# Kernel tuning notes

Hardware: AMD Instinct MI355X
Metric: run time of the kernel (lower is better)

The kernel has to match this reference:

```python
import jax, jax.numpy as jnp
import numpy as np

D_MODEL = 1024
D_FF = 4096
N_EXPERTS = 8
TOP_K = 2

def setup_inputs() -> dict:
    key = jax.random.key(0)
    ks = jax.random.split(key, 8)
    s = 0.02
    return {
        "x": jax.random.normal(ks[0], (4, 2048, D_MODEL), dtype=jnp.float32),
        "W1": jax.random.normal(ks[1], (N_EXPERTS, D_MODEL, D_FF), dtype=jnp.float32) * s,
        "b1": jnp.zeros((N_EXPERTS, D_FF), dtype=jnp.float32),
        "W2": jax.random.normal(ks[2], (N_EXPERTS, D_FF, D_MODEL), dtype=jnp.float32) * s,
        "b2": jnp.zeros((N_EXPERTS, D_MODEL), dtype=jnp.float32),
        "Wg": jax.random.normal(ks[3], (D_MODEL, N_EXPERTS), dtype=jnp.float32) * s,
        "bg": jnp.zeros((N_EXPERTS,), dtype=jnp.float32),
    }

def reference(x, W1, b1, W2, b2, Wg, bg):
    B, S, D = x.shape
    # Gating network
    gate_logits = jnp.einsum('bsd,de->bse', x, Wg) + bg
    gate_probs = jax.nn.softmax(gate_logits, axis=-1)  # (B,S,E)
    # Top-k routing on softmax probs (matches torch.topk(F.softmax(logits)))
    top_k_probs, top_k_indices = jax.lax.top_k(gate_probs, TOP_K)  # (B,S,k)
    T = B * S
    x_flat = x.reshape(T, D)
    idx_flat = top_k_indices.reshape(T, TOP_K)
    prob_flat = top_k_probs.reshape(T, TOP_K)
    # Per-token combine weight for each expert: sum of top-k probs routed to it
    # combine[t, e] = sum_j prob_flat[t, j] * (idx_flat[t, j] == e)
    onehot = jax.nn.one_hot(idx_flat, N_EXPERTS, dtype=x.dtype)  # (T,k,E)
    combine = jnp.einsum('tk,tke->te', prob_flat, onehot)  # (T,E)
    out = jnp.zeros((T, D), dtype=x.dtype)
    for e in range(N_EXPERTS):  # static small loop over experts
        h = jax.nn.relu(x_flat @ W1[e] + b1[e])  # (T, d_ff)
        y = h @ W2[e] + b2[e]                    # (T, d_model)
        out = out + combine[:, e:e+1] * y
    return out.reshape(B, S, D), gate_probs
```

## Files before the change

kernel.cpp:

```cpp
#include <hip/hip_runtime.h>

#define D_MODEL 1024
#define D_FF    4096
#define N_EXP   8
#define BM 128
#define BN 128
#define BK 32

typedef __attribute__((ext_vector_type(8))) short bf16x8;
typedef __attribute__((ext_vector_type(4))) float f32x4;
typedef unsigned int u32;

__device__ __forceinline__ unsigned short f2bf(float f) {
  union { float f; unsigned u; } v; v.f = f;
  unsigned r = v.u + 0x7FFFu + ((v.u >> 16) & 1u);
  return (unsigned short)(r >> 16);
}

__device__ __forceinline__ void gl_lds16(const void* g, void* l) {
  __builtin_amdgcn_global_load_lds((const __attribute__((address_space(1))) u32*)g,
                                   (__attribute__((address_space(3))) u32*)l, 16, 0, 0);
}

__global__ __launch_bounds__(256)
void transpose_convert_all(const float* __restrict__ W1, const float* __restrict__ W2,
                           unsigned short* __restrict__ w1t, unsigned short* __restrict__ w2t) {
  __shared__ u32 s32k[32][65];
  int z = blockIdx.z;
  const float* se;
  unsigned short* de;
  int Ksub, Nsrc, kb, nb;
  if (z < 8) {
    Ksub = D_MODEL; Nsrc = D_FF;
    kb = blockIdx.y * 64; nb = blockIdx.x * 64;
    se = W1 + (size_t)z * D_MODEL * D_FF;
    de = w1t + (size_t)z * D_FF * D_MODEL;
  } else {
    Ksub = D_FF; Nsrc = D_MODEL;
    kb = blockIdx.x * 64; nb = blockIdx.y * 64;
    se = W2 + (size_t)(z - 8) * D_FF * D_MODEL;
    de = w2t + (size_t)(z - 8) * D_MODEL * D_FF;
  }
  se += (size_t)kb * Nsrc + nb;
  de += (size_t)nb * Ksub + kb;
  int tid = threadIdx.x;
  int kh = tid >> 4;
  int n4 = (tid & 15) * 4;
  #pragma unroll
  for (int p = 0; p < 2; p++) {
    int k = kh * 2 + p * 32;
    float4 v0 = *(const float4*)(se + (size_t)k * Nsrc + n4);
    float4 v1 = *(const float4*)(se + (size_t)(k + 1) * Nsrc + n4);
    #pragma unroll
    for (int j = 0; j < 4; j++) {
      u32 pk = (u32)f2bf(((const float*)&v0)[j]) |
               ((u32)f2bf(((const float*)&v1)[j]) << 16);
      s32k[k >> 1][n4 + j] = pk;
    }
  }
  __syncthreads();
  #pragma unroll
  for (int c = 0; c < 2; c++) {
    int id = tid + c * 256;
    int n = id >> 3, kc = id & 7;
    uint4 o;
    o.x = s32k[kc * 4 + 0][n];
    o.y = s32k[kc * 4 + 1][n];
    o.z = s32k[kc * 4 + 2][n];
    o.w = s32k[kc * 4 + 3][n];
    *(uint4*)(de + (size_t)n * Ksub + kc * 8) = o;
  }
}

__global__ void gating_kernel(const float* __restrict__ x,
                              const float* __restrict__ Wg,
                              const float* __restrict__ bg,
                              float* __restrict__ gate_out,
                              unsigned short* __restrict__ xb,
                              int* __restrict__ cnt,
                              int* __restrict__ tokIdx,
                              float* __restrict__ tokW, int T) {
  int wv = threadIdx.x >> 6, lane = threadIdx.x & 63;
  int t = blockIdx.x * 4 + wv;
  if (t >= T) return;
  const float* xr = x + (size_t)t * D_MODEL + lane * 16;
  float acc[N_EXP];
  #pragma unroll
  for (int e = 0; e < N_EXP; e++) acc[e] = 0.f;
  ushort4 xc[4];
  #pragma unroll
  for (int q = 0; q < 4; q++) {
    float4 xv = *(const float4*)(xr + q * 4);
    xc[q].x = f2bf(xv.x); xc[q].y = f2bf(xv.y);
    xc[q].z = f2bf(xv.z); xc[q].w = f2bf(xv.w);
    #pragma unroll
    for (int r = 0; r < 4; r++) {
      float xs = ((const float*)&xv)[r];
      const float* wrow = Wg + (size_t)(lane * 16 + q * 4 + r) * N_EXP;
      float4 wa = *(const float4*)wrow;
      float4 wb = *(const float4*)(wrow + 4);
      acc[0] += xs * wa.x; acc[1] += xs * wa.y; acc[2] += xs * wa.z; acc[3] += xs * wa.w;
      acc[4] += xs * wb.x; acc[5] += xs * wb.y; acc[6] += xs * wb.z; acc[7] += xs * wb.w;
    }
  }
  unsigned short* xbr = xb + (size_t)t * D_MODEL + lane * 16;
  #pragma unroll
  for (int q = 0; q < 4; q++) *(ushort4*)(xbr + q * 4) = xc[q];
  #pragma unroll
  for (int off = 32; off > 0; off >>= 1) {
    #pragma unroll
    for (int e = 0; e < N_EXP; e++) acc[e] += __shfl_xor(acc[e], off);
  }
  if (lane == 0) {
    float l[N_EXP], p[N_EXP];
    float m = -1e30f;
    #pragma unroll
    for (int e = 0; e < N_EXP; e++) { l[e] = acc[e] + bg[e]; m = fmaxf(m, l[e]); }
    float s = 0.f;
    #pragma unroll
    for (int e = 0; e < N_EXP; e++) { p[e] = __expf(l[e] - m); s += p[e]; }
    float inv = 1.f / s;
    #pragma unroll
    for (int e = 0; e < N_EXP; e++) { p[e] *= inv; gate_out[(size_t)t * N_EXP + e] = p[e]; }
    int e1 = 0;
    #pragma unroll
    for (int e = 1; e < N_EXP; e++) if (p[e] > p[e1]) e1 = e;
    int e2 = (e1 == 0) ? 1 : 0;
    #pragma unroll
    for (int e = 0; e < N_EXP; e++) if (e != e1 && p[e] > p[e2]) e2 = e;
    int pos = atomicAdd(cnt + e1, 1);
    tokIdx[(size_t)e1 * T + pos] = t; tokW[(size_t)e1 * T + pos] = p[e1];
    pos = atomicAdd(cnt + e2, 1);
    tokIdx[(size_t)e2 * T + pos] = t; tokW[(size_t)e2 * T + pos] = p[e2];
  }
}

__global__ void schedule_kernel(const int* __restrict__ cnt, int* __restrict__ meta,
                                int* __restrict__ tE, int* __restrict__ tB,
                                int* __restrict__ tV, int T, int maxTiles) {
  if (threadIdx.x != 0 || blockIdx.x != 0) return;
  int t = 0;
  for (int e = 0; e < N_EXP; e++) {
    int c = cnt[e];
    for (int r = 0; r < c && t < maxTiles; r += BM) {
      tE[t] = e; tB[t] = e * T + r; tV[t] = min(BM, c - r); t++;
    }
  }
  meta[0] = t;
}

#define STAGE(b, kt) { _Pragma("unroll") for (int p_ = 0; p_ < 2; p_++) { \
    gl_lds16(srcA[p_] + (size_t)(kt) * BK, &LDSU[(b) * 8192 + (w * 32 + p_ * 16) * 32]); \
    gl_lds16(srcB[p_] + (size_t)(kt) * BK, &LDSU[(b) * 8192 + 4096 + (w * 32 + p_ * 16) * 32]); } }

#define COMPUTE(b) { \
    bf16x8 ra[4], rb[4]; \
    _Pragma("unroll") for (int m_ = 0; m_ < 4; m_++) { \
      int row_ = wr * 64 + m_ * 16 + l15; \
      ra[m_] = *(const bf16x8*)&LDSU[(b) * 8192 + row_ * 32 + (((l4 + (row_ >> 1)) & 3) << 3)]; } \
    _Pragma("unroll") for (int n_ = 0; n_ < 4; n_++) { \
      int rb_ = wc * 64 + n_ * 16 + l15; \
      rb[n_] = *(const bf16x8*)&LDSU[(b) * 8192 + 4096 + rb_ * 32 + (((l4 + (rb_ >> 1)) & 3) << 3)]; } \
    _Pragma("unroll") for (int m_ = 0; m_ < 4; m_++) \
      _Pragma("unroll") for (int n_ = 0; n_ < 4; n_++) \
        acc[m_][n_] = __builtin_amdgcn_mfma_f32_16x16x32_bf16(ra[m_], rb[n_], acc[m_][n_], 0, 0, 0); }

#define BAR() { __builtin_amdgcn_s_barrier(); asm volatile("" ::: "memory"); }
#define WAITVM(N) asm volatile("s_waitcnt vmcnt(" #N ")" ::: "memory");

#define PIPE3(NT) \
  STAGE(0, 0); STAGE(1, 1); \
  for (int it = 0; it < ((NT) - 2) / 3; it++) { \
    int kt = 3 * it; \
    STAGE(2, kt + 2); WAITVM(8); BAR(); COMPUTE(0); BAR(); \
    STAGE(0, kt + 3); WAITVM(8); BAR(); COMPUTE(1); BAR(); \
    STAGE(1, kt + 4); WAITVM(8); BAR(); COMPUTE(2); BAR(); \
  } \
  WAITVM(4); BAR(); COMPUTE(0); BAR(); \
  WAITVM(0); BAR(); COMPUTE(1);

__global__ __launch_bounds__(256)
void gemm1_kernel(const unsigned short* __restrict__ xb,
                  const unsigned short* __restrict__ w1t,
                  const float* __restrict__ b1,
                  const int* __restrict__ meta,
                  const int* __restrict__ tE, const int* __restrict__ tB,
                  const int* __restrict__ tV, const int* __restrict__ tokIdx,
                  unsigned short* __restrict__ h, int nT) {
  __shared__ unsigned short LDSU[24576];

  int total = gridDim.x;
  int L = blockIdx.x;
  int q = total >> 3, r8 = total & 7;
  int xcd = L & 7, idx = L >> 3;
  int work = (xcd < r8) ? (xcd * (q + 1) + idx) : (r8 * (q + 1) + (xcd - r8) * q + idx);
  int cb = work / nT;
  int tile = work - cb * nT;
  if (tile >= meta[0]) return;
  int e = tE[tile], base = tB[tile], valid = tV[tile];
  int tid = threadIdx.x;

  int w = tid >> 6, lane = tid & 63;
  int wr = w >> 1, wc = w & 1;
  int l15 = lane & 15, l4 = lane >> 4;
  int lrow = lane >> 2, lch = lane & 3;

  const unsigned short* panel = w1t + (size_t)e * D_FF * D_MODEL;
  const unsigned short* srcA[2];
  const unsigned short* srcB[2];
  #pragma unroll
  for (int p = 0; p < 2; p++) {
    int r = w * 32 + p * 16 + lrow;
    int tok = tokIdx[base + (r < valid ? r : valid - 1)];
    int g = (lch - (r >> 1)) & 3;
    srcA[p] = xb + (size_t)tok * D_MODEL + g * 8;
    srcB[p] = panel + (size_t)(cb * BN + r) * D_MODEL + g * 8;
  }

  f32x4 acc[4][4];
  #pragma unroll
  for (int m = 0; m < 4; m++)
    #pragma unroll
    for (int n = 0; n < 4; n++) acc[m][n] = (f32x4){0.f, 0.f, 0.f, 0.f};

  PIPE3(D_MODEL / BK);

  #pragma unroll
  for (int n = 0; n < 4; n++) {
    int colc = cb * BN + wc * 64 + n * 16 + l15;
    float bias = b1[(size_t)e * D_FF + colc];
    #pragma unroll
    for (int m = 0; m < 4; m++) {
      #pragma unroll
      for (int r = 0; r < 4; r++) {
        int row = wr * 64 + m * 16 + l4 * 4 + r;
        float v = acc[m][n][r] + bias;
        v = v > 0.f ? v : 0.f;
        h[(size_t)(tile * BM + row) * D_FF + colc] = f2bf(v);
      }
    }
  }
}

__global__ __launch_bounds__(256)
void gemm2_kernel(const unsigned short* __restrict__ h,
                  const unsigned short* __restrict__ w2t,
                  const float* __restrict__ b2,
                  const int* __restrict__ meta,
                  const int* __restrict__ tE, const int* __restrict__ tB,
                  const int* __restrict__ tV, const int* __restrict__ tokIdx,
                  const float* __restrict__ tokW,
                  float* __restrict__ out) {
  __shared__ unsigned short LDSU[24576];

  int total = gridDim.x;
  int L = blockIdx.x;
  int q = total >> 3, r8 = total & 7;
  int xcd = L & 7, idx = L >> 3;
  int work = (xcd < r8) ? (xcd * (q + 1) + idx) : (r8 * (q + 1) + (xcd - r8) * q + idx);
  int tile = work >> 3;
  int cb = work & 7;
  if (tile >= meta[0]) return;
  int e = tE[tile], base = tB[tile], valid = tV[tile];
  int tid = threadIdx.x;

  int w = tid >> 6, lane = tid & 63;
  int wr = w >> 1, wc = w & 1;
  int l15 = lane & 15, l4 = lane >> 4;
  int lrow = lane >> 2, lch = lane & 3;

  const unsigned short* panel = w2t + (size_t)e * D_MODEL * D_FF;
  const unsigned short* srcA[2];
  const unsigned short* srcB[2];
  #pragma unroll
  for (int p = 0; p < 2; p++) {
    int r = w * 32 + p * 16 + lrow;
    int g = (lch - (r >> 1)) & 3;
    srcA[p] = h + (size_t)(tile * BM + r) * D_FF + g * 8;
    srcB[p] = panel + (size_t)(cb * BN + r) * D_FF + g * 8;
  }

  f32x4 acc[4][4];
  #pragma unroll
  for (int m = 0; m < 4; m++)
    #pragma unroll
    for (int n = 0; n < 4; n++) acc[m][n] = (f32x4){0.f, 0.f, 0.f, 0.f};

  PIPE3(D_FF / BK);

  float biasv[4];
  #pragma unroll
  for (int n = 0; n < 4; n++)
    biasv[n] = b2[(size_t)e * D_MODEL + cb * BN + wc * 64 + n * 16 + l15];

  #pragma unroll
  for (int m = 0; m < 4; m++) {
    #pragma unroll
    for (int r = 0; r < 4; r++) {
      int row = wr * 64 + m * 16 + l4 * 4 + r;
      if (row < valid) {
        int tok = tokIdx[base + row];
        float wgt = tokW[base + row];
        float* orow = out + (size_t)tok * D_MODEL + cb * BN + wc * 64 + l15;
        #pragma unroll
        for (int n = 0; n < 4; n++)
          atomicAdd(orow + n * 16, (acc[m][n][r] + biasv[n]) * wgt);
      }
    }
  }
}

extern "C" void kernel_launch(void* const* d_in, const int* in_sizes, int n_in,
                              void* d_out, int out_size, void* d_ws, size_t ws_size,
                              hipStream_t stream) {
  const float* x  = (const float*)d_in[0];
  const float* W1 = (const float*)d_in[1];
  const float* b1 = (const float*)d_in[2];
  const float* W2 = (const float*)d_in[3];
  const float* b2 = (const float*)d_in[4];
  const float* Wg = (const float*)d_in[5];
  const float* bg = (const float*)d_in[6];

  int T = in_sizes[0] / D_MODEL;
  float* out = (float*)d_out;
  float* gate_out = out + (size_t)T * D_MODEL;

  char* ws = (char*)d_ws;
  int* cnt  = (int*)(ws + 0);
  int* meta = (int*)(ws + 64);
  int* tE   = (int*)(ws + 128);
  int* tB   = (int*)(ws + 1024);
  int* tV   = (int*)(ws + 2048);
  size_t off = 4096;
  int* tokIdx = (int*)(ws + off);   off += (size_t)N_EXP * T * 4;
  float* tokW = (float*)(ws + off); off += (size_t)N_EXP * T * 4;
  unsigned short* xb = (unsigned short*)(ws + off); off += (size_t)T * D_MODEL * 2;
  off = (off + 255) & ~(size_t)255;

  int maxTiles = (2 * T) / BM + N_EXP;

  unsigned short* w1t = (unsigned short*)(ws + off); off += (size_t)N_EXP * D_MODEL * D_FF * 2;
  unsigned short* w2t = (unsigned short*)(ws + off); off += (size_t)N_EXP * D_MODEL * D_FF * 2;
  unsigned short* h   = (unsigned short*)(ws + off);

  hipMemsetAsync(d_out, 0, (size_t)T * D_MODEL * sizeof(float), stream);
  hipMemsetAsync(cnt, 0, N_EXP * sizeof(int), stream);

  gating_kernel<<<(T + 3) / 4, 256, 0, stream>>>(x, Wg, bg, gate_out, xb, cnt, tokIdx, tokW, T);
  schedule_kernel<<<1, 64, 0, stream>>>(cnt, meta, tE, tB, tV, T, maxTiles);

  transpose_convert_all<<<dim3(64, 16, 16), 256, 0, stream>>>(W1, W2, w1t, w2t);

  gemm1_kernel<<<maxTiles * (D_FF / BN), 256, 0, stream>>>(
      xb, w1t, b1, meta, tE, tB, tV, tokIdx, h, maxTiles);
  gemm2_kernel<<<maxTiles * (D_MODEL / BN), 256, 0, stream>>>(
      h, w2t, b2, meta, tE, tB, tV, tokIdx, tokW, out);
}
```

Measured before the change: 738.9 us.

## Use 512-thread blocks with 2x4 wave grid for expert GEMMs

Both expert GEMM kernels now run 8 waves per block in a 2x4 arrangement instead of 4 waves in 2x2, so each wave computes a 64x32 sub-tile with half the accumulators. Each thread issues one global-to-LDS load per operand per stage, and the vmcnt waits are adjusted to match. This lowers per-thread register pressure and adds latency hiding within the same 128x128 tile, at the cost of more redundant A-fragment LDS reads per MFMA and heavier barrier synchronization across 8 waves.

```diff
diff --git a/kernel.cpp b/kernel.cpp
--- a/kernel.cpp
+++ b/kernel.cpp
@@ -149,21 +149,21 @@
   meta[0] = t;
 }
 
-#define STAGE(b, kt) { _Pragma("unroll") for (int p_ = 0; p_ < 2; p_++) { \
-    gl_lds16(srcA[p_] + (size_t)(kt) * BK, &LDSU[(b) * 8192 + (w * 32 + p_ * 16) * 32]); \
-    gl_lds16(srcB[p_] + (size_t)(kt) * BK, &LDSU[(b) * 8192 + 4096 + (w * 32 + p_ * 16) * 32]); } }
+#define STAGE(b, kt) { \
+    gl_lds16(srcA0 + (size_t)(kt) * BK, &LDSU[(b) * 8192 + w * 512]); \
+    gl_lds16(srcB0 + (size_t)(kt) * BK, &LDSU[(b) * 8192 + 4096 + w * 512]); }
 
 #define COMPUTE(b) { \
-    bf16x8 ra[4], rb[4]; \
+    bf16x8 ra[4], rbv[2]; \
     _Pragma("unroll") for (int m_ = 0; m_ < 4; m_++) { \
       int row_ = wr * 64 + m_ * 16 + l15; \
       ra[m_] = *(const bf16x8*)&LDSU[(b) * 8192 + row_ * 32 + (((l4 + (row_ >> 1)) & 3) << 3)]; } \
-    _Pragma("unroll") for (int n_ = 0; n_ < 4; n_++) { \
-      int rb_ = wc * 64 + n_ * 16 + l15; \
-      rb[n_] = *(const bf16x8*)&LDSU[(b) * 8192 + 4096 + rb_ * 32 + (((l4 + (rb_ >> 1)) & 3) << 3)]; } \
+    _Pragma("unroll") for (int n_ = 0; n_ < 2; n_++) { \
+      int rb_ = wc * 32 + n_ * 16 + l15; \
+      rbv[n_] = *(const bf16x8*)&LDSU[(b) * 8192 + 4096 + rb_ * 32 + (((l4 + (rb_ >> 1)) & 3) << 3)]; } \
     _Pragma("unroll") for (int m_ = 0; m_ < 4; m_++) \
-      _Pragma("unroll") for (int n_ = 0; n_ < 4; n_++) \
-        acc[m_][n_] = __builtin_amdgcn_mfma_f32_16x16x32_bf16(ra[m_], rb[n_], acc[m_][n_], 0, 0, 0); }
+      _Pragma("unroll") for (int n_ = 0; n_ < 2; n_++) \
+        acc[m_][n_] = __builtin_amdgcn_mfma_f32_16x16x32_bf16(ra[m_], rbv[n_], acc[m_][n_], 0, 0, 0); }
 
 #define BAR() { __builtin_amdgcn_s_barrier(); asm volatile("" ::: "memory"); }
 #define WAITVM(N) asm volatile("s_waitcnt vmcnt(" #N ")" ::: "memory");
@@ -172,14 +172,18 @@
   STAGE(0, 0); STAGE(1, 1); \
   for (int it = 0; it < ((NT) - 2) / 3; it++) { \
     int kt = 3 * it; \
-    STAGE(2, kt + 2); WAITVM(8); BAR(); COMPUTE(0); BAR(); \
-    STAGE(0, kt + 3); WAITVM(8); BAR(); COMPUTE(1); BAR(); \
-    STAGE(1, kt + 4); WAITVM(8); BAR(); COMPUTE(2); BAR(); \
+    STAGE(2, kt + 2); WAITVM(4); BAR(); COMPUTE(0); BAR(); \
+    STAGE(0, kt + 3); WAITVM(4); BAR(); COMPUTE(1); BAR(); \
+    STAGE(1, kt + 4); WAITVM(4); BAR(); COMPUTE(2); BAR(); \
   } \
-  WAITVM(4); BAR(); COMPUTE(0); BAR(); \
+  WAITVM(2); BAR(); COMPUTE(0); BAR(); \
   WAITVM(0); BAR(); COMPUTE(1);
 
-__global__ __launch_bounds__(256)
+#define ACC_INIT() f32x4 acc[4][2]; \
+  _Pragma("unroll") for (int m = 0; m < 4; m++) \
+    _Pragma("unroll") for (int n = 0; n < 2; n++) acc[m][n] = (f32x4){0.f, 0.f, 0.f, 0.f};
+
+__global__ __launch_bounds__(512)
 void gemm1_kernel(const unsigned short* __restrict__ xb,
                   const unsigned short* __restrict__ w1t,
                   const float* __restrict__ b1,
@@ -201,33 +205,23 @@
   int tid = threadIdx.x;
 
   int w = tid >> 6, lane = tid & 63;
-  int wr = w >> 1, wc = w & 1;
+  int wr = w >> 2, wc = w & 3;
   int l15 = lane & 15, l4 = lane >> 4;
-  int lrow = lane >> 2, lch = lane & 3;
+  int sr = lane >> 2, lch = lane & 3;
 
   const unsigned short* panel = w1t + (size_t)e * D_FF * D_MODEL;
-  const unsigned short* srcA[2];
-  const unsigned short* srcB[2];
-  #pragma unroll
-  for (int p = 0; p < 2; p++) {
-    int r = w * 32 + p * 16 + lrow;
-    int tok = tokIdx[base + (r < valid ? r : valid - 1)];
-    int g = (lch - (r >> 1)) & 3;
-    srcA[p] = xb + (size_t)tok * D_MODEL + g * 8;
-    srcB[p] = panel + (size_t)(cb * BN + r) * D_MODEL + g * 8;
-  }
-
-  f32x4 acc[4][4];
-  #pragma unroll
-  for (int m = 0; m < 4; m++)
-    #pragma unroll
-    for (int n = 0; n < 4; n++) acc[m][n] = (f32x4){0.f, 0.f, 0.f, 0.f};
-
+  int rS = w * 16 + sr;
+  int tokS = tokIdx[base + (rS < valid ? rS : valid - 1)];
+  int g = (lch - (rS >> 1)) & 3;
+  const unsigned short* srcA0 = xb + (size_t)tokS * D_MODEL + g * 8;
+  const unsigned short* srcB0 = panel + (size_t)(cb * BN + rS) * D_MODEL + g * 8;
+
+  ACC_INIT();
   PIPE3(D_MODEL / BK);
 
   #pragma unroll
-  for (int n = 0; n < 4; n++) {
-    int colc = cb * BN + wc * 64 + n * 16 + l15;
+  for (int n = 0; n < 2; n++) {
+    int colc = cb * BN + wc * 32 + n * 16 + l15;
     float bias = b1[(size_t)e * D_FF + colc];
     #pragma unroll
     for (int m = 0; m < 4; m++) {
@@ -242,7 +236,7 @@
   }
 }
 
-__global__ __launch_bounds__(256)
+__global__ __launch_bounds__(512)
 void gemm2_kernel(const unsigned short* __restrict__ h,
                   const unsigned short* __restrict__ w2t,
                   const float* __restrict__ b2,
@@ -265,33 +259,23 @@
   int tid = threadIdx.x;
 
   int w = tid >> 6, lane = tid & 63;
-  int wr = w >> 1, wc = w & 1;
+  int wr = w >> 2, wc = w & 3;
   int l15 = lane & 15, l4 = lane >> 4;
-  int lrow = lane >> 2, lch = lane & 3;
+  int sr = lane >> 2, lch = lane & 3;
 
   const unsigned short* panel = w2t + (size_t)e * D_MODEL * D_FF;
-  const unsigned short* srcA[2];
-  const unsigned short* srcB[2];
-  #pragma unroll
-  for (int p = 0; p < 2; p++) {
-    int r = w * 32 + p * 16 + lrow;
-    int g = (lch - (r >> 1)) & 3;
-    srcA[p] = h + (size_t)(tile * BM + r) * D_FF + g * 8;
-    srcB[p] = panel + (size_t)(cb * BN + r) * D_FF + g * 8;
-  }
-
-  f32x4 acc[4][4];
-  #pragma unroll
-  for (int m = 0; m < 4; m++)
-    #pragma unroll
-    for (int n = 0; n < 4; n++) acc[m][n] = (f32x4){0.f, 0.f, 0.f, 0.f};
-
+  int rS = w * 16 + sr;
+  int g = (lch - (rS >> 1)) & 3;
+  const unsigned short* srcA0 = h + (size_t)(tile * BM + rS) * D_FF + g * 8;
+  const unsigned short* srcB0 = panel + (size_t)(cb * BN + rS) * D_FF + g * 8;
+
+  ACC_INIT();
   PIPE3(D_FF / BK);
 
-  float biasv[4];
-  #pragma unroll
-  for (int n = 0; n < 4; n++)
-    biasv[n] = b2[(size_t)e * D_MODEL + cb * BN + wc * 64 + n * 16 + l15];
+  float biasv[2];
+  #pragma unroll
+  for (int n = 0; n < 2; n++)
+    biasv[n] = b2[(size_t)e * D_MODEL + cb * BN + wc * 32 + n * 16 + l15];
 
   #pragma unroll
   for (int m = 0; m < 4; m++) {
@@ -301,9 +285,9 @@
       if (row < valid) {
         int tok = tokIdx[base + row];
         float wgt = tokW[base + row];
-        float* orow = out + (size_t)tok * D_MODEL + cb * BN + wc * 64 + l15;
+        float* orow = out + (size_t)tok * D_MODEL + cb * BN + wc * 32 + l15;
         #pragma unroll
-        for (int n = 0; n < 4; n++)
+        for (int n = 0; n < 2; n++)
           atomicAdd(orow + n * 16, (acc[m][n][r] + biasv[n]) * wgt);
       }
     }
@@ -351,8 +335,8 @@
 
   transpose_convert_all<<<dim3(64, 16, 16), 256, 0, stream>>>(W1, W2, w1t, w2t);
 
-  gemm1_kernel<<<maxTiles * (D_FF / BN), 256, 0, stream>>>(
+  gemm1_kernel<<<maxTiles * (D_FF / BN), 512, 0, stream>>>(
       xb, w1t, b1, meta, tE, tB, tV, tokIdx, h, maxTiles);
-  gemm2_kernel<<<maxTiles * (D_MODEL / BN), 256, 0, stream>>>(
+  gemm2_kernel<<<maxTiles * (D_MODEL / BN), 512, 0, stream>>>(
       h, w2t, b2, meta, tE, tB, tV, tokIdx, tokW, out);
 }
```

Result: faster. 710.8 us (-3.8%).
